# Kernel optimization log

Hardware: AMD Instinct MI355X
Metric: run time of the kernel (lower is better)

The kernel has to match this reference:

```python
import jax, jax.numpy as jnp
import numpy as np


def _grid_sample_2d(feat, gx, gy):
    """Bilinear grid sample, zeros padding, align_corners=False.
    feat: [B,C,H,W]; gx,gy: [B,S,h,w] normalized coords in [-1,1].
    Returns [B,C,S,h,w]. Matches torch 5D grid_sample with D=1, z=0
    (z pixel coord = (1*1-1)/2 = 0 -> weight 1 on the single depth slice).
    """
    B, C, H, W = feat.shape
    ix = ((gx + 1.0) * W - 1.0) * 0.5  # unnormalize, align_corners=False
    iy = ((gy + 1.0) * H - 1.0) * 0.5
    x0 = jnp.floor(ix)
    y0 = jnp.floor(iy)
    tx = ix - x0  # fractional parts (differentiable w.r.t. grid)
    ty = iy - y0
    x0i = x0.astype(jnp.int32)
    y0i = y0.astype(jnp.int32)
    feat_flat = feat.reshape(B, C, H * W)

    def gather(xi, yi):
        valid = (xi >= 0) & (xi < W) & (yi >= 0) & (yi < H)
        xc = jnp.clip(xi, 0, W - 1)
        yc = jnp.clip(yi, 0, H - 1)
        idx = (yc * W + xc).reshape(B, 1, -1)  # [B,1,S*h*w]
        g = jnp.take_along_axis(feat_flat, idx, axis=2)  # [B,C,S*h*w]
        g = g.reshape(B, C, *xi.shape[1:])  # [B,C,S,h,w]
        return g * valid.astype(feat.dtype)[:, None]

    v00 = gather(x0i, y0i)
    v01 = gather(x0i + 1, y0i)
    v10 = gather(x0i, y0i + 1)
    v11 = gather(x0i + 1, y0i + 1)
    w00 = ((1.0 - tx) * (1.0 - ty))[:, None]
    w01 = (tx * (1.0 - ty))[:, None]
    w10 = ((1.0 - tx) * ty)[:, None]
    w11 = (tx * ty)[:, None]
    return v00 * w00 + v01 * w01 + v10 * w10 + v11 * w11


def setup_inputs() -> dict:
    key = jax.random.key(0)
    k1, k2, k3, k4 = jax.random.split(key, 4)
    B, C, S, H, W = 8, 8, 16, 128, 416
    feat_l = jax.random.normal(k1, (B, C, H, W), dtype=jnp.float32)
    feat_r = jax.random.normal(k2, (B, C, H, W), dtype=jnp.float32)
    # LUT: x,y normalized coords (slightly beyond [-1,1] to exercise zero padding);
    # z channel fixed to 0 exactly as in the module's lut_batch construction.
    lut_xy = jax.random.uniform(k3, (B, S, H, W, 2), dtype=jnp.float32,
                                minval=-1.1, maxval=1.1)
    lut = jnp.concatenate([lut_xy, jnp.zeros((B, S, H, W, 1), jnp.float32)], axis=-1)
    valid_mask = jax.random.bernoulli(k4, 0.8, (B, C, S, H, W))
    return {"feat_l": feat_l, "feat_r": feat_r, "lut": lut,
            "valid_mask": valid_mask, "no_steps": S}


def reference(feat_l, feat_r, lut, valid_mask, no_steps):
    """AnyNet._build_volume_2d: LUT grid_sample warp + masked inf-fill
    + abs-diff + channel-sum cost volume. Returns [B, no_steps, H, W]."""
    gx = lut[..., 0]  # torch grid order: (x, y, z), x indexes width
    gy = lut[..., 1]
    warped = _grid_sample_2d(feat_r, gx, gy)          # [B,C,S,H,W]
    diff = jnp.abs(warped - feat_l[:, :, None])       # broadcast feat_l over S
    cost_disp_feat = jnp.where(valid_mask, diff, jnp.inf)
    cost_volume = jnp.sum(cost_disp_feat, axis=1)     # [B,S,H,W]
    return cost_volume
```

## Files before the change

### kernel.cpp

```cpp
#include <hip/hip_runtime.h>
#include <math.h>

#define BB 8
#define CC 8
#define SS 16
#define HH 128
#define WW 416
#define HWSZ (HH * WW)
#define WP1 (WW + 1)

typedef unsigned short u16;
typedef unsigned char  u8;
typedef unsigned short ushort8 __attribute__((ext_vector_type(8)));

__device__ __forceinline__ float bf2f(u16 v) {
    union { unsigned int u; float f; } x;
    x.u = ((unsigned int)v) << 16;
    return x.f;
}

__device__ __forceinline__ u16 f2bf(float f) {
    union { float ff; unsigned int u; } x;
    x.ff = f;
    unsigned int lsb = (x.u >> 16) & 1u;
    return (u16)((x.u + 0x7FFFu + lsb) >> 16);
}

__global__ __launch_bounds__(256) void pack_feat_r_rep(
    const u16* __restrict__ feat_r, u16* __restrict__ pr)
{
    const int idx = blockIdx.x * 256 + threadIdx.x;
    const int b = idx / (HH * WP1);
    const int rem = idx - b * (HH * WP1);
    const int y = rem / WP1;
    const int e = rem - y * WP1;
    const int xa = min(max(e - 1, 0), WW - 1);
    const int xb = min(e, WW - 1);

    const size_t src = ((size_t)b * CC * HH + y) * WW;
    ushort8 va, vb;
#pragma unroll
    for (int c = 0; c < CC; ++c) {
        va[c] = feat_r[src + (size_t)c * HH * WW + xa];
        vb[c] = feat_r[src + (size_t)c * HH * WW + xb];
    }
    ushort8* dst = (ushort8*)(pr + (size_t)idx * 16);
    dst[0] = va;
    dst[1] = vb;
}

__global__ __launch_bounds__(256) void pack_feat_l(
    const u16* __restrict__ feat_l, ushort8* __restrict__ pl)
{
    const int idx = blockIdx.x * 256 + threadIdx.x;
    const int b = idx / HWSZ;
    const int p = idx - b * HWSZ;
    const size_t base = (size_t)b * CC * HWSZ + p;
    ushort8 v;
#pragma unroll
    for (int c = 0; c < CC; ++c) v[c] = feat_l[base + (size_t)c * HWSZ];
    pl[idx] = v;
}

__global__ __launch_bounds__(256) void anynet_cost_volume(
    const u16* __restrict__ pfr,
    const ushort8* __restrict__ pfl,
    const u16* __restrict__ lut,
    const u8*  __restrict__ vmask,
    u16* __restrict__ out)
{
    const int hw = blockIdx.x * 256 + threadIdx.x;
    const int bs = blockIdx.y;
    const int s  = bs & (SS - 1);
    const int b  = bs >> 4;

    const size_t loff = ((size_t)bs * HWSZ + hw) * 3;
    const float gx = bf2f(lut[loff + 0]);
    const float gy = bf2f(lut[loff + 1]);

    const float ix = ((gx + 1.0f) * (float)WW - 1.0f) * 0.5f;
    const float iy = ((gy + 1.0f) * (float)HH - 1.0f) * 0.5f;
    const float x0f = floorf(ix);
    const float y0f = floorf(iy);
    const float tx = ix - x0f;
    const float ty = iy - y0f;
    const int x0 = (int)x0f;
    const int y0 = (int)y0f;
    const int x1 = x0 + 1;
    const int y1 = y0 + 1;

    const bool vx0 = ((unsigned)x0 < (unsigned)WW);
    const bool vx1 = ((unsigned)x1 < (unsigned)WW);
    const bool vy0 = ((unsigned)y0 < (unsigned)HH);
    const bool vy1 = ((unsigned)y1 < (unsigned)HH);

    const int yc0 = min(max(y0, 0), HH - 1);
    const int yc1 = min(max(y1, 0), HH - 1);
    const int ec = min(max(x0 + 1, 0), WW);

    const float w00 = (1.0f - tx) * (1.0f - ty) * ((vx0 && vy0) ? 1.0f : 0.0f);
    const float w01 = tx * (1.0f - ty)          * ((vx1 && vy0) ? 1.0f : 0.0f);
    const float w10 = (1.0f - tx) * ty          * ((vx0 && vy1) ? 1.0f : 0.0f);
    const float w11 = tx * ty                   * ((vx1 && vy1) ? 1.0f : 0.0f);

    const u16* r0 = pfr + (((size_t)b * HH + yc0) * WP1 + ec) * 16;
    const u16* r1 = pfr + (((size_t)b * HH + yc1) * WP1 + ec) * 16;
    const ushort8 p00 = ((const ushort8*)r0)[0];
    const ushort8 p01 = ((const ushort8*)r0)[1];
    const ushort8 p10 = ((const ushort8*)r1)[0];
    const ushort8 p11 = ((const ushort8*)r1)[1];
    const ushort8 fl8 = pfl[(size_t)b * HWSZ + hw];

    const u8* __restrict__ vm = vmask + ((size_t)(b * CC) * SS + s) * HWSZ + hw;

    float acc = 0.0f;
    bool any_invalid = false;
#pragma unroll
    for (int c = 0; c < CC; ++c) {
        const float warped = bf2f(p00[c]) * w00 + bf2f(p01[c]) * w01
                           + bf2f(p10[c]) * w10 + bf2f(p11[c]) * w11;
        const float d = fabsf(warped - bf2f(fl8[c]));
        any_invalid |= (vm[(size_t)c * SS * HWSZ] == 0);
        acc += d;
    }

    acc = fminf(fmaxf(acc, 0.0f), 1e30f);
    if (!(acc >= 0.0f && acc <= 1e30f)) acc = 0.0f;
    out[(size_t)bs * HWSZ + hw] = any_invalid ? (u16)0x7F7F : f2bf(acc);
}

extern "C" void kernel_launch(void* const* d_in, const int* in_sizes, int n_in,
                              void* d_out, int out_size, void* d_ws, size_t ws_size,
                              hipStream_t stream) {
    const u16* feat_l = (const u16*)d_in[0];
    const u16* feat_r = (const u16*)d_in[1];
    const u16* lut    = (const u16*)d_in[2];
    const u8*  vmask  = (const u8*)d_in[3];
    u16* out = (u16*)d_out;

    u16* pfr = (u16*)d_ws;
    ushort8* pfl = (ushort8*)(pfr + (size_t)BB * HH * WP1 * 16);

    pack_feat_r_rep<<<dim3(BB * HH * WP1 / 256), dim3(256), 0, stream>>>(feat_r, pfr);
    pack_feat_l<<<dim3(BB * HWSZ / 256), dim3(256), 0, stream>>>(feat_l, pfl);

    dim3 grid(HWSZ / 256, BB * SS);
    anynet_cost_volume<<<grid, dim3(256), 0, stream>>>(pfr, pfl, lut, vmask, out);
}
```

Measured before the change: 345.6 us.

## Process two pixels per thread with wider loads and fuse packing kernels

The main cost-volume kernel now handles two adjacent pixels per thread. It reads the LUT as three 32-bit words, reads the mask bytes as 16-bit pairs, and writes the two bf16 outputs with one 32-bit store, which cuts the number of narrow memory transactions. The two pre-packing kernels are merged into one launch with a two-row grid, saving one launch. The cost is more register pressure and half as many threads in the main kernel, so less latency hiding for the gathers.

```diff
diff --git a/kernel.cpp b/kernel.cpp
--- a/kernel.cpp
+++ b/kernel.cpp
@@ -11,73 +11,55 @@
 
 typedef unsigned short u16;
 typedef unsigned char  u8;
+typedef unsigned int   u32;
 typedef unsigned short ushort8 __attribute__((ext_vector_type(8)));
 
 __device__ __forceinline__ float bf2f(u16 v) {
-    union { unsigned int u; float f; } x;
-    x.u = ((unsigned int)v) << 16;
-    return x.f;
+    union { u32 u; float f; } x; x.u = ((u32)v) << 16; return x.f;
 }
-
 __device__ __forceinline__ u16 f2bf(float f) {
-    union { float ff; unsigned int u; } x;
-    x.ff = f;
-    unsigned int lsb = (x.u >> 16) & 1u;
+    union { float ff; u32 u; } x; x.ff = f;
+    u32 lsb = (x.u >> 16) & 1u;
     return (u16)((x.u + 0x7FFFu + lsb) >> 16);
 }
 
-__global__ __launch_bounds__(256) void pack_feat_r_rep(
-    const u16* __restrict__ feat_r, u16* __restrict__ pr)
+__global__ __launch_bounds__(256) void pack_all(
+    const u16* __restrict__ feat_l, const u16* __restrict__ feat_r,
+    u16* __restrict__ pr, ushort8* __restrict__ pl)
 {
     const int idx = blockIdx.x * 256 + threadIdx.x;
-    const int b = idx / (HH * WP1);
-    const int rem = idx - b * (HH * WP1);
-    const int y = rem / WP1;
-    const int e = rem - y * WP1;
-    const int xa = min(max(e - 1, 0), WW - 1);
-    const int xb = min(e, WW - 1);
-
-    const size_t src = ((size_t)b * CC * HH + y) * WW;
-    ushort8 va, vb;
+    if (blockIdx.y == 0) {
+        const int b = idx / (HH * WP1);
+        const int rem = idx - b * (HH * WP1);
+        const int y = rem / WP1;
+        const int e = rem - y * WP1;
+        const int xa = min(max(e - 1, 0), WW - 1);
+        const int xb = min(e, WW - 1);
+        const size_t src = ((size_t)b * CC * HH + y) * WW;
+        ushort8 va, vb;
 #pragma unroll
-    for (int c = 0; c < CC; ++c) {
-        va[c] = feat_r[src + (size_t)c * HH * WW + xa];
-        vb[c] = feat_r[src + (size_t)c * HH * WW + xb];
+        for (int c = 0; c < CC; ++c) {
+            va[c] = feat_r[src + (size_t)c * HH * WW + xa];
+            vb[c] = feat_r[src + (size_t)c * HH * WW + xb];
+        }
+        ushort8* dst = (ushort8*)(pr + (size_t)idx * 16);
+        dst[0] = va; dst[1] = vb;
+    } else {
+        if (idx >= BB * HWSZ) return;
+        const int b = idx / HWSZ;
+        const int p = idx - b * HWSZ;
+        const size_t base = (size_t)b * CC * HWSZ + p;
+        ushort8 v;
+#pragma unroll
+        for (int c = 0; c < CC; ++c) v[c] = feat_l[base + (size_t)c * HWSZ];
+        pl[idx] = v;
     }
-    ushort8* dst = (ushort8*)(pr + (size_t)idx * 16);
-    dst[0] = va;
-    dst[1] = vb;
 }
 
-__global__ __launch_bounds__(256) void pack_feat_l(
-    const u16* __restrict__ feat_l, ushort8* __restrict__ pl)
+__device__ __forceinline__ void corner_setup(
+    float gx, float gy, int& ec, int& yc0, int& yc1,
+    float& w00, float& w01, float& w10, float& w11)
 {
-    const int idx = blockIdx.x * 256 + threadIdx.x;
-    const int b = idx / HWSZ;
-    const int p = idx - b * HWSZ;
-    const size_t base = (size_t)b * CC * HWSZ + p;
-    ushort8 v;
-#pragma unroll
-    for (int c = 0; c < CC; ++c) v[c] = feat_l[base + (size_t)c * HWSZ];
-    pl[idx] = v;
-}
-
-__global__ __launch_bounds__(256) void anynet_cost_volume(
-    const u16* __restrict__ pfr,
-    const ushort8* __restrict__ pfl,
-    const u16* __restrict__ lut,
-    const u8*  __restrict__ vmask,
-    u16* __restrict__ out)
-{
-    const int hw = blockIdx.x * 256 + threadIdx.x;
-    const int bs = blockIdx.y;
-    const int s  = bs & (SS - 1);
-    const int b  = bs >> 4;
-
-    const size_t loff = ((size_t)bs * HWSZ + hw) * 3;
-    const float gx = bf2f(lut[loff + 0]);
-    const float gy = bf2f(lut[loff + 1]);
-
     const float ix = ((gx + 1.0f) * (float)WW - 1.0f) * 0.5f;
     const float iy = ((gy + 1.0f) * (float)HH - 1.0f) * 0.5f;
     const float x0f = floorf(ix);
@@ -86,47 +68,84 @@
     const float ty = iy - y0f;
     const int x0 = (int)x0f;
     const int y0 = (int)y0f;
-    const int x1 = x0 + 1;
-    const int y1 = y0 + 1;
+    const bool vx0 = ((unsigned)x0 < (unsigned)WW);
+    const bool vx1 = ((unsigned)(x0 + 1) < (unsigned)WW);
+    const bool vy0 = ((unsigned)y0 < (unsigned)HH);
+    const bool vy1 = ((unsigned)(y0 + 1) < (unsigned)HH);
+    yc0 = min(max(y0, 0), HH - 1);
+    yc1 = min(max(y0 + 1, 0), HH - 1);
+    ec  = min(max(x0 + 1, 0), WW);
+    w00 = (1.0f - tx) * (1.0f - ty) * ((vx0 && vy0) ? 1.0f : 0.0f);
+    w01 = tx * (1.0f - ty)          * ((vx1 && vy0) ? 1.0f : 0.0f);
+    w10 = (1.0f - tx) * ty          * ((vx0 && vy1) ? 1.0f : 0.0f);
+    w11 = tx * ty                   * ((vx1 && vy1) ? 1.0f : 0.0f);
+}
 
-    const bool vx0 = ((unsigned)x0 < (unsigned)WW);
-    const bool vx1 = ((unsigned)x1 < (unsigned)WW);
-    const bool vy0 = ((unsigned)y0 < (unsigned)HH);
-    const bool vy1 = ((unsigned)y1 < (unsigned)HH);
+__global__ __launch_bounds__(256) void anynet_cost_volume2(
+    const u16* __restrict__ pfr,
+    const ushort8* __restrict__ pfl,
+    const u16* __restrict__ lut,
+    const u8*  __restrict__ vmask,
+    u16* __restrict__ out)
+{
+    const int t  = blockIdx.x * 256 + threadIdx.x;
+    const int hw0 = t * 2;
+    const int bs = blockIdx.y;
+    const int s  = bs & (SS - 1);
+    const int b  = bs >> 4;
 
-    const int yc0 = min(max(y0, 0), HH - 1);
-    const int yc1 = min(max(y1, 0), HH - 1);
-    const int ec = min(max(x0 + 1, 0), WW);
+    const u32* lp = (const u32*)(lut + ((size_t)bs * HWSZ + hw0) * 3);
+    const u32 u0 = lp[0];
+    const u32 u1 = lp[1];
+    const u32 u2 = lp[2];
+    const float gxA = bf2f((u16)(u0 & 0xFFFFu));
+    const float gyA = bf2f((u16)(u0 >> 16));
+    const float gxB = bf2f((u16)(u1 >> 16));
+    const float gyB = bf2f((u16)(u2 & 0xFFFFu));
 
-    const float w00 = (1.0f - tx) * (1.0f - ty) * ((vx0 && vy0) ? 1.0f : 0.0f);
-    const float w01 = tx * (1.0f - ty)          * ((vx1 && vy0) ? 1.0f : 0.0f);
-    const float w10 = (1.0f - tx) * ty          * ((vx0 && vy1) ? 1.0f : 0.0f);
-    const float w11 = tx * ty                   * ((vx1 && vy1) ? 1.0f : 0.0f);
+    int ecA, y0A, y1A, ecB, y0B, y1B;
+    float w00A, w01A, w10A, w11A, w00B, w01B, w10B, w11B;
+    corner_setup(gxA, gyA, ecA, y0A, y1A, w00A, w01A, w10A, w11A);
+    corner_setup(gxB, gyB, ecB, y0B, y1B, w00B, w01B, w10B, w11B);
 
-    const u16* r0 = pfr + (((size_t)b * HH + yc0) * WP1 + ec) * 16;
-    const u16* r1 = pfr + (((size_t)b * HH + yc1) * WP1 + ec) * 16;
-    const ushort8 p00 = ((const ushort8*)r0)[0];
-    const ushort8 p01 = ((const ushort8*)r0)[1];
-    const ushort8 p10 = ((const ushort8*)r1)[0];
-    const ushort8 p11 = ((const ushort8*)r1)[1];
-    const ushort8 fl8 = pfl[(size_t)b * HWSZ + hw];
+    const size_t bhp = (size_t)b * HH;
+    const ushort8* rA0 = (const ushort8*)(pfr + ((bhp + y0A) * WP1 + ecA) * 16);
+    const ushort8* rA1 = (const ushort8*)(pfr + ((bhp + y1A) * WP1 + ecA) * 16);
+    const ushort8* rB0 = (const ushort8*)(pfr + ((bhp + y0B) * WP1 + ecB) * 16);
+    const ushort8* rB1 = (const ushort8*)(pfr + ((bhp + y1B) * WP1 + ecB) * 16);
+    const ushort8 pA00 = rA0[0], pA01 = rA0[1];
+    const ushort8 pA10 = rA1[0], pA11 = rA1[1];
+    const ushort8 pB00 = rB0[0], pB01 = rB0[1];
+    const ushort8 pB10 = rB1[0], pB11 = rB1[1];
 
-    const u8* __restrict__ vm = vmask + ((size_t)(b * CC) * SS + s) * HWSZ + hw;
+    const ushort8 flA = pfl[(size_t)b * HWSZ + hw0];
+    const ushort8 flB = pfl[(size_t)b * HWSZ + hw0 + 1];
 
-    float acc = 0.0f;
-    bool any_invalid = false;
+    const u8* __restrict__ vm = vmask + ((size_t)(b * CC) * SS + s) * HWSZ + hw0;
+
+    float accA = 0.0f, accB = 0.0f;
+    bool invA = false, invB = false;
 #pragma unroll
     for (int c = 0; c < CC; ++c) {
-        const float warped = bf2f(p00[c]) * w00 + bf2f(p01[c]) * w01
-                           + bf2f(p10[c]) * w10 + bf2f(p11[c]) * w11;
-        const float d = fabsf(warped - bf2f(fl8[c]));
-        any_invalid |= (vm[(size_t)c * SS * HWSZ] == 0);
-        acc += d;
+        const float wA = bf2f(pA00[c]) * w00A + bf2f(pA01[c]) * w01A
+                       + bf2f(pA10[c]) * w10A + bf2f(pA11[c]) * w11A;
+        const float wB = bf2f(pB00[c]) * w00B + bf2f(pB01[c]) * w01B
+                       + bf2f(pB10[c]) * w10B + bf2f(pB11[c]) * w11B;
+        accA += fabsf(wA - bf2f(flA[c]));
+        accB += fabsf(wB - bf2f(flB[c]));
+        const u16 m2 = *(const u16*)(vm + (size_t)c * SS * HWSZ);
+        invA |= ((m2 & 0x00FFu) == 0);
+        invB |= ((m2 & 0xFF00u) == 0);
     }
 
-    acc = fminf(fmaxf(acc, 0.0f), 1e30f);
-    if (!(acc >= 0.0f && acc <= 1e30f)) acc = 0.0f;
-    out[(size_t)bs * HWSZ + hw] = any_invalid ? (u16)0x7F7F : f2bf(acc);
+    accA = fminf(fmaxf(accA, 0.0f), 1e30f);
+    accB = fminf(fmaxf(accB, 0.0f), 1e30f);
+    if (!(accA >= 0.0f && accA <= 1e30f)) accA = 0.0f;
+    if (!(accB >= 0.0f && accB <= 1e30f)) accB = 0.0f;
+    const u32 oA = invA ? 0x7F7Fu : (u32)f2bf(accA);
+    const u32 oB = invB ? 0x7F7Fu : (u32)f2bf(accB);
+
+    *(u32*)(out + (size_t)bs * HWSZ + hw0) = oA | (oB << 16);
 }
 
 extern "C" void kernel_launch(void* const* d_in, const int* in_sizes, int n_in,
@@ -141,9 +160,9 @@
     u16* pfr = (u16*)d_ws;
     ushort8* pfl = (ushort8*)(pfr + (size_t)BB * HH * WP1 * 16);
 
-    pack_feat_r_rep<<<dim3(BB * HH * WP1 / 256), dim3(256), 0, stream>>>(feat_r, pfr);
-    pack_feat_l<<<dim3(BB * HWSZ / 256), dim3(256), 0, stream>>>(feat_l, pfl);
+    pack_all<<<dim3(BB * HH * WP1 / 256, 2), dim3(256), 0, stream>>>(
+        feat_l, feat_r, pfr, pfl);
 
-    dim3 grid(HWSZ / 256, BB * SS);
-    anynet_cost_volume<<<grid, dim3(256), 0, stream>>>(pfr, pfl, lut, vmask, out);
+    dim3 grid(HWSZ / 2 / 256, BB * SS);
+    anynet_cost_volume2<<<grid, dim3(256), 0, stream>>>(pfr, pfl, lut, vmask, out);
 }
```

Measured after the change: 353.4 us. 1.02x slower.
